# Kernel tuning notes

Hardware: AMD Instinct MI355X
Metric: run time of the kernel (lower is better)

## Reference

```python
import jax, jax.numpy as jnp
import numpy as np

B, L, H, DI, N, R, K = 1, 1024, 2048, 4096, 16, 128, 4


def setup_inputs() -> dict:
    key = jax.random.key(0)
    ks = jax.random.split(key, 12)
    s = 0.02
    x = jax.random.normal(ks[0], (B, L, H), jnp.float32)
    W_in_states = jax.random.normal(ks[1], (DI, H), jnp.float32) * s
    W_in_gates = jax.random.normal(ks[2], (DI, H), jnp.float32) * s
    conv_w = jax.random.normal(ks[3], (DI, K), jnp.float32) * 0.2
    conv_b = jax.random.normal(ks[4], (DI,), jnp.float32) * 0.02
    W_dt = jax.random.normal(ks[5], (R, DI), jnp.float32) * s
    W_b = jax.random.normal(ks[6], (N, DI), jnp.float32) * s
    W_c = jax.random.normal(ks[7], (N, DI), jnp.float32) * s
    W_dtproj = jax.random.normal(ks[8], (DI, R), jnp.float32) * 0.1
    # dt bias so softplus(dt) is in a realistic small range
    b_dtproj = jax.random.uniform(ks[9], (DI,), jnp.float32, minval=-5.0, maxval=-3.0)
    A_log = jnp.log(jnp.broadcast_to(jnp.arange(1, N + 1, dtype=jnp.float32), (DI, N)))
    D = jnp.ones((DI,), jnp.float32)
    W_out = jax.random.normal(ks[10], (H, DI), jnp.float32) * s
    return {"x": x, "W_in_states": W_in_states, "W_in_gates": W_in_gates,
            "conv_w": conv_w, "conv_b": conv_b, "W_dt": W_dt, "W_b": W_b,
            "W_c": W_c, "W_dtproj": W_dtproj, "b_dtproj": b_dtproj,
            "A_log": A_log, "D": D, "W_out": W_out}


def _silu(v):
    return v * jax.nn.sigmoid(v)


def reference(x, W_in_states, W_in_gates, conv_w, conv_b, W_dt, W_b, W_c,
              W_dtproj, b_dtproj, A_log, D, W_out):
    b, l, _ = x.shape
    # input projections -> [B, DI, L]
    hs = jnp.einsum('blh,dh->bdl', x, W_in_states)
    gate = jnp.einsum('blh,dh->bdl', x, W_in_gates)
    # causal depthwise conv1d (kernel K, left pad K-1, truncate to L)
    k = conv_w.shape[-1]
    xpad = jnp.pad(hs, ((0, 0), (0, 0), (k - 1, 0)))
    conv = sum(conv_w[None, :, j, None] * xpad[:, :, j:j + l] for j in range(k))
    conv = conv + conv_b[None, :, None]
    hs = _silu(conv)                       # [B, DI, L]
    hst = hs.transpose(0, 2, 1)            # [B, L, DI]
    # data-dependent SSM params
    time_step = jnp.einsum('bld,rd->blr', hst, W_dt)           # [B, L, R]
    dt = jax.nn.softplus(time_step @ W_dtproj.T + b_dtproj)    # [B, L, DI]
    Bm = jnp.einsum('bld,nd->bln', hst, W_b)                   # [B, L, N]
    Cm = jnp.einsum('bld,nd->bln', hst, W_c)                   # [B, L, N]
    A = -jnp.exp(A_log)                                        # [DI, N]
    dt_bdl = dt.transpose(0, 2, 1)                             # [B, DI, L]
    dA = jnp.exp(A[None, :, None, :] * dt_bdl[:, :, :, None])  # [B, DI, L, N]
    dBu = dt_bdl[:, :, :, None] * Bm[:, None, :, :] * hs[:, :, :, None]
    # sequential selective scan over L
    dA_l = dA.transpose(2, 0, 1, 3)    # [L, B, DI, N]
    dBu_l = dBu.transpose(2, 0, 1, 3)

    def step(s, inp):
        a, bu = inp
        s = a * s + bu
        return s, s

    init = jnp.zeros((b, hs.shape[1], A_log.shape[1]), hs.dtype)
    _, h = jax.lax.scan(step, init, (dA_l, dBu_l))   # [L, B, DI, N]
    y = jnp.einsum('lbdn,bln->bdl', h, Cm)           # contract state dim
    y = y + hs * D[None, :, None]
    y = y * _silu(gate)
    out = jnp.einsum('bdl,od->blo', y, W_out)        # [B, L, H]
    return out
```

## Files before the change

kernel.cpp:

```cpp
#include <hip/hip_runtime.h>

#define SEQ 1024
#define HID 2048
#define DIN 4096
#define NST 16
#define RNK 128
#define CHN 64
#define CLEN 16

typedef __attribute__((ext_vector_type(4))) float f32x4;
typedef __attribute__((ext_vector_type(4))) __bf16 bf16x4v;
typedef __attribute__((ext_vector_type(8))) __bf16 bf16x8v;
typedef __attribute__((ext_vector_type(8))) unsigned short u16x8;

#define GPTR(p) ((const __attribute__((address_space(1))) void*)(p))
#define LPTR(p) ((__attribute__((address_space(3))) void*)(p))

__device__ __forceinline__ unsigned short f2bf(float v) {
  unsigned u = __builtin_bit_cast(unsigned, v);
  u = (u + 0x7fffu + ((u >> 16) & 1u)) >> 16;
  return (unsigned short)u;
}
__device__ __forceinline__ float softplus_f(float x) {
  return (x > 20.f) ? x : log1pf(__expf(x));
}
__device__ __forceinline__ float silu_f(float x) {
  return x / (1.f + __expf(-x));
}

#define CV_NX  (SEQ*HID)
#define CV_NW  (DIN*HID)
#define CV_NDT (RNK*DIN)
#define CV_NB  (NST*DIN)
#define CV_NPD (32*DIN)
#define CV_NWO (HID*DIN)
#define CV_TOT (CV_NX + 2*CV_NW + CV_NDT + 2*CV_NB + CV_NPD + CV_NDT + CV_NWO)

__global__ __launch_bounds__(256) void cvt_all(
    const float* __restrict__ x, const float* __restrict__ wis,
    const float* __restrict__ wig, const float* __restrict__ wdt,
    const float* __restrict__ wb, const float* __restrict__ wc,
    const float* __restrict__ wdtp, const float* __restrict__ wout,
    unsigned short* __restrict__ x_bf, unsigned short* __restrict__ wis_bf,
    unsigned short* __restrict__ wig_bf, unsigned short* __restrict__ wcat_bf,
    unsigned short* __restrict__ wdtp_bf, unsigned short* __restrict__ wout_bf)
{
  size_t j = ((size_t)blockIdx.x * 256 + threadIdx.x) * 8;
  const float* src = nullptr; unsigned short* dst;
  if (j < CV_NX) { src = x + j; dst = x_bf + j; }
  else if ((j -= CV_NX) < CV_NW) { src = wis + j; dst = wis_bf + j; }
  else if ((j -= CV_NW) < CV_NW) { src = wig + j; dst = wig_bf + j; }
  else if ((j -= CV_NW) < CV_NDT) { src = wdt + j; dst = wcat_bf + j; }
  else if ((j -= CV_NDT) < CV_NB) { src = wb + j; dst = wcat_bf + (size_t)128*DIN + j; }
  else if ((j -= CV_NB) < CV_NB) { src = wc + j; dst = wcat_bf + (size_t)144*DIN + j; }
  else if ((j -= CV_NB) < CV_NPD) { dst = wcat_bf + (size_t)160*DIN + j; }
  else if ((j -= CV_NPD) < CV_NDT) { src = wdtp + j; dst = wdtp_bf + j; }
  else { j -= CV_NDT; src = wout + j; dst = wout_bf + j; }
  u16x8 o = {};
  if (src) {
    f32x4 a = *(const f32x4*)src;
    f32x4 b = *(const f32x4*)(src + 4);
#pragma unroll
    for (int i = 0; i < 4; i++) { o[i] = f2bf(a[i]); o[4 + i] = f2bf(b[i]); }
  }
  *(u16x8*)dst = o;
}

template<int EPI>
__global__ __launch_bounds__(256) void gemm128(
    const unsigned short* __restrict__ Ag, const unsigned short* __restrict__ Bg,
    float* __restrict__ Cg, const float* __restrict__ bias,
    int Msz, int Nsz, int Kstride, int Kiter)
{
  __shared__ __align__(16) unsigned short As[2][128 * 64];
  __shared__ __align__(16) unsigned short Bs[2][128 * 64];
  const int kz = blockIdx.z;
  Ag += (size_t)kz * Kiter;
  Bg += (size_t)kz * Kiter;
  Cg += (size_t)kz * Msz * Nsz;
  const int nwg = gridDim.x * gridDim.y;
  const int orig = blockIdx.y * gridDim.x + blockIdx.x;
  const int swz = (orig & 7) * (nwg >> 3) + (orig >> 3);
  const int bx = swz % gridDim.x, by = swz / gridDim.x;
  const int tid = threadIdx.x;
  const int m0 = bx * 128, n0 = by * 128;
  const int lane = tid & 63, w = tid >> 6;
  const int wm = w >> 1, wn = w & 1;
  const int lg = lane >> 4, lr = lane & 15;
  const int srow = w * 32 + (lane >> 3);
  const int sslot = (lane & 7) ^ (lane >> 3);
  const unsigned short* Ag0 = Ag + (size_t)(m0 + srow) * Kstride + sslot * 8;
  const unsigned short* Bg0 = Bg + (size_t)(n0 + srow) * Kstride + sslot * 8;
  const int ldso = w * 2048;

  auto stage = [&](int b, int k0) {
#pragma unroll
    for (int i = 0; i < 4; i++)
      __builtin_amdgcn_global_load_lds(GPTR(Ag0 + (size_t)(i * 8) * Kstride + k0),
                                       LPTR(&As[b][ldso + i * 512]), 16, 0, 0);
#pragma unroll
    for (int i = 0; i < 4; i++)
      __builtin_amdgcn_global_load_lds(GPTR(Bg0 + (size_t)(i * 8) * Kstride + k0),
                                       LPTR(&Bs[b][ldso + i * 512]), 16, 0, 0);
  };

  const int nt = Kiter >> 6;
  stage(0, 0);
  f32x4 acc[4][4] = {};
  int cur = 0;
  const int rsw = lr & 7;
  for (int t = 0; t < nt; ++t) {
    asm volatile("s_waitcnt vmcnt(0)" ::: "memory");
    __builtin_amdgcn_s_barrier();
    asm volatile("" ::: "memory");
    if (t + 1 < nt) stage(cur ^ 1, (t + 1) * 64);
    bf16x8v af0[4], bf0[4], af1[4], bf1[4];
#pragma unroll
    for (int mi = 0; mi < 4; mi++) {
      const int row = (wm * 64 + mi * 16 + lr) * 64;
      af0[mi] = *(const bf16x8v*)&As[cur][row + ((0 * 4 + lg) ^ rsw) * 8];
      af1[mi] = *(const bf16x8v*)&As[cur][row + ((1 * 4 + lg) ^ rsw) * 8];
    }
#pragma unroll
    for (int ni = 0; ni < 4; ni++) {
      const int row = (wn * 64 + ni * 16 + lr) * 64;
      bf0[ni] = *(const bf16x8v*)&Bs[cur][row + ((0 * 4 + lg) ^ rsw) * 8];
      bf1[ni] = *(const bf16x8v*)&Bs[cur][row + ((1 * 4 + lg) ^ rsw) * 8];
    }
#pragma unroll
    for (int mi = 0; mi < 4; mi++)
#pragma unroll
      for (int ni = 0; ni < 4; ni++)
        acc[mi][ni] = __builtin_amdgcn_mfma_f32_16x16x32_bf16(af0[mi], bf0[ni], acc[mi][ni], 0, 0, 0);
#pragma unroll
    for (int mi = 0; mi < 4; mi++)
#pragma unroll
      for (int ni = 0; ni < 4; ni++)
        acc[mi][ni] = __builtin_amdgcn_mfma_f32_16x16x32_bf16(af1[mi], bf1[ni], acc[mi][ni], 0, 0, 0);
    cur ^= 1;
  }
#pragma unroll
  for (int mi = 0; mi < 4; mi++) {
#pragma unroll
    for (int ni = 0; ni < 4; ni++) {
      const int col = n0 + wn * 64 + ni * 16 + lr;
#pragma unroll
      for (int r = 0; r < 4; r++) {
        const int row = m0 + wm * 64 + mi * 16 + lg * 4 + r;
        float v = acc[mi][ni][r];
        if (EPI == 1) v = softplus_f(v + bias[col]);
        Cg[(size_t)row * Nsz + col] = v;
      }
    }
  }
}

template<int EPI>
__global__ __launch_bounds__(256) void gemm_nt(
    const unsigned short* __restrict__ Ag, const unsigned short* __restrict__ Bg,
    float* __restrict__ Cg, const float* __restrict__ bias,
    int Msz, int Nsz, int Kstride, int Kiter)
{
  __shared__ __align__(16) unsigned short As[128][40];
  __shared__ __align__(16) unsigned short Bs[64][40];
  const int kz = blockIdx.z;
  Ag += (size_t)kz * Kiter;
  Bg += (size_t)kz * Kiter;
  Cg += (size_t)kz * Msz * Nsz;
  const int tid = threadIdx.x;
  const int m0 = blockIdx.x * 128, n0 = blockIdx.y * 64;
  const int lane = tid & 63, w = tid >> 6;
  const int wm = w >> 1, wn = w & 1;
  const int lg = lane >> 4, lr = lane & 15;
  const int r4 = tid >> 2, c8 = (tid & 3) * 8;
  f32x4 acc[4][2] = {};
  for (int k0 = 0; k0 < Kiter; k0 += 32) {
    uint4 a0 = *(const uint4*)(Ag + (size_t)(m0 + r4) * Kstride + k0 + c8);
    uint4 a1 = *(const uint4*)(Ag + (size_t)(m0 + 64 + r4) * Kstride + k0 + c8);
    uint4 b0 = *(const uint4*)(Bg + (size_t)(n0 + r4) * Kstride + k0 + c8);
    *(uint4*)&As[r4][c8] = a0;
    *(uint4*)&As[64 + r4][c8] = a1;
    *(uint4*)&Bs[r4][c8] = b0;
    __syncthreads();
    bf16x8v af[4], bfr[2];
#pragma unroll
    for (int mi = 0; mi < 4; mi++) {
      const int row = wm * 64 + mi * 16 + lr;
      bf16x4v lo = *(const bf16x4v*)&As[row][4 * lg];
      bf16x4v hi = *(const bf16x4v*)&As[row][16 + 4 * lg];
      af[mi] = __builtin_shufflevector(lo, hi, 0, 1, 2, 3, 4, 5, 6, 7);
    }
#pragma unroll
    for (int ni = 0; ni < 2; ni++) {
      const int row = wn * 32 + ni * 16 + lr;
      bf16x4v lo = *(const bf16x4v*)&Bs[row][4 * lg];
      bf16x4v hi = *(const bf16x4v*)&Bs[row][16 + 4 * lg];
      bfr[ni] = __builtin_shufflevector(lo, hi, 0, 1, 2, 3, 4, 5, 6, 7);
    }
#pragma unroll
    for (int mi = 0; mi < 4; mi++)
#pragma unroll
      for (int ni = 0; ni < 2; ni++)
        acc[mi][ni] = __builtin_amdgcn_mfma_f32_16x16x32_bf16(af[mi], bfr[ni], acc[mi][ni], 0, 0, 0);
    __syncthreads();
  }
#pragma unroll
  for (int mi = 0; mi < 4; mi++) {
#pragma unroll
    for (int ni = 0; ni < 2; ni++) {
      const int col = n0 + wn * 32 + ni * 16 + lr;
#pragma unroll
      for (int r = 0; r < 4; r++) {
        const int row = m0 + wm * 64 + mi * 16 + lg * 4 + r;
        float v = acc[mi][ni][r];
        if (EPI == 1) v = softplus_f(v + bias[col]);
        Cg[(size_t)row * Nsz + col] = v;
      }
    }
  }
}

__global__ __launch_bounds__(256) void conv_silu(
    const float* __restrict__ pg, const float* __restrict__ cw,
    const float* __restrict__ cb, float* __restrict__ hs,
    unsigned short* __restrict__ hs_bf)
{
  int idx = blockIdx.x * 256 + threadIdx.x;
  int l = idx >> 12, d = idx & (DIN - 1);
  float acc = cb[d];
#pragma unroll
  for (int j = 0; j < 4; j++) {
    int ll = l + j - 3;
    float v = (ll >= 0) ? pg[(size_t)ll * 8192 + d] : 0.f;
    acc = fmaf(cw[d * 4 + j], v, acc);
  }
  float r = silu_f(acc);
  hs[idx] = r;
  hs_bf[idx] = f2bf(r);
}

__global__ __launch_bounds__(256) void reduce_ts(
    const float* __restrict__ c2p, float* __restrict__ c2,
    unsigned short* __restrict__ ts_bf)
{
  int i = blockIdx.x * 256 + threadIdx.x;
  float s = 0.f;
#pragma unroll
  for (int z = 0; z < 8; z++) s += c2p[(size_t)z * SEQ * 192 + i];
  c2[i] = s;
  int l = i / 192, col = i - l * 192;
  if (col < 128) ts_bf[l * 128 + col] = f2bf(s);
}

__global__ __launch_bounds__(256) void reduce_out(
    const float* __restrict__ p, float* __restrict__ out)
{
  int i = (blockIdx.x * 256 + threadIdx.x) * 4;
  float4 a = *(const float4*)&p[i];
#pragma unroll
  for (int z = 1; z < 4; z++) {
    float4 b = *(const float4*)&p[(size_t)z * SEQ * HID + i];
    a.x += b.x; a.y += b.y; a.z += b.z; a.w += b.w;
  }
  *(float4*)&out[i] = a;
}

__global__ __launch_bounds__(256) void scan_phase1(
    const float* __restrict__ dt, const float* __restrict__ hs,
    const float* __restrict__ c2, const float* __restrict__ alog,
    float* __restrict__ Pbuf, float* __restrict__ Sbuf)
{
  __shared__ float B_ch[CLEN][16];
  const int tid = threadIdx.x;
  const int d = blockIdx.x * 256 + tid;
  const int c = blockIdx.y;
  const int l0 = c * CLEN;
  B_ch[tid >> 4][tid & 15] = c2[(size_t)(l0 + (tid >> 4)) * 192 + 128 + (tid & 15)];
  float a[16];
#pragma unroll
  for (int i = 0; i < 16; i++) a[i] = -__expf(alog[(size_t)d * 16 + i]);
  __syncthreads();
  float s[16] = {};
  float P[16];
#pragma unroll
  for (int i = 0; i < 16; i++) P[i] = 1.f;
  for (int t = 0; t < CLEN; t++) {
    float dtv = dt[(size_t)(l0 + t) * DIN + d];
    float u = hs[(size_t)(l0 + t) * DIN + d];
    float w = dtv * u;
#pragma unroll
    for (int n = 0; n < 16; n++) {
      float dA = __expf(a[n] * dtv);
      s[n] = fmaf(dA, s[n], w * B_ch[t][n]);
      P[n] *= dA;
    }
  }
  size_t base = ((size_t)c * DIN + d) * 16;
#pragma unroll
  for (int i = 0; i < 4; i++) {
    *(float4*)&Sbuf[base + 4 * i] = *(float4*)&s[4 * i];
    *(float4*)&Pbuf[base + 4 * i] = *(float4*)&P[4 * i];
  }
}

__global__ __launch_bounds__(256) void scan_phase2(
    const float* __restrict__ Pbuf, float* __restrict__ Sbuf)
{
  size_t idx = (size_t)blockIdx.x * 256 + threadIdx.x;
  const size_t stride = (size_t)DIN * 16;
  float s = 0.f;
#pragma unroll 4
  for (int c = 0; c < CHN; c++) {
    float Pv = Pbuf[c * stride + idx];
    float Sv = Sbuf[c * stride + idx];
    Sbuf[c * stride + idx] = s;
    s = fmaf(Pv, s, Sv);
  }
}

__global__ __launch_bounds__(256) void scan_phase3(
    const float* __restrict__ dt, const float* __restrict__ hs,
    const float* __restrict__ pg, const float* __restrict__ c2,
    const float* __restrict__ alog, const float* __restrict__ Dv,
    const float* __restrict__ sig, unsigned short* __restrict__ ygT)
{
  __shared__ float B_ch[CLEN][16], C_ch[CLEN][16];
  const int tid = threadIdx.x;
  const int d = blockIdx.x * 256 + tid;
  const int c = blockIdx.y;
  const int l0 = c * CLEN;
  {
    int t = tid >> 4, n = tid & 15;
    B_ch[t][n] = c2[(size_t)(l0 + t) * 192 + 128 + n];
    C_ch[t][n] = c2[(size_t)(l0 + t) * 192 + 144 + n];
  }
  float a[16];
#pragma unroll
  for (int i = 0; i < 16; i++) a[i] = -__expf(alog[(size_t)d * 16 + i]);
  const float Dd = Dv[d];
  float s[16];
  size_t base = ((size_t)c * DIN + d) * 16;
#pragma unroll
  for (int i = 0; i < 4; i++) *(float4*)&s[4 * i] = *(const float4*)&sig[base + 4 * i];
  __syncthreads();
  for (int t = 0; t < CLEN; t++) {
    float dtv = dt[(size_t)(l0 + t) * DIN + d];
    float u = hs[(size_t)(l0 + t) * DIN + d];
    float g = pg[(size_t)(l0 + t) * 8192 + 4096 + d];
    float w = dtv * u;
    float y = 0.f;
#pragma unroll
    for (int n = 0; n < 16; n++) {
      float dA = __expf(a[n] * dtv);
      s[n] = fmaf(dA, s[n], w * B_ch[t][n]);
      y = fmaf(s[n], C_ch[t][n], y);
    }
    float o = (y + u * Dd) * silu_f(g);
    ygT[(size_t)(l0 + t) * DIN + d] = f2bf(o);
  }
}

extern "C" void kernel_launch(void* const* d_in, const int* in_sizes, int n_in,
                              void* d_out, int out_size, void* d_ws, size_t ws_size,
                              hipStream_t stream) {
  const float* x     = (const float*)d_in[0];
  const float* wis   = (const float*)d_in[1];
  const float* wig   = (const float*)d_in[2];
  const float* convw = (const float*)d_in[3];
  const float* convb = (const float*)d_in[4];
  const float* wdt   = (const float*)d_in[5];
  const float* wb    = (const float*)d_in[6];
  const float* wc    = (const float*)d_in[7];
  const float* wdtp  = (const float*)d_in[8];
  const float* bdtp  = (const float*)d_in[9];
  const float* alog  = (const float*)d_in[10];
  const float* Dv    = (const float*)d_in[11];
  const float* wout  = (const float*)d_in[12];

  char* ws = (char*)d_ws;
  size_t off = 0;
  auto alloc = [&](size_t bytes) { void* p = ws + off; off += (bytes + 255) & ~(size_t)255; return p; };
  unsigned short* x_bf    = (unsigned short*)alloc((size_t)SEQ * HID * 2);
  unsigned short* wis_bf  = (unsigned short*)alloc((size_t)DIN * HID * 2);
  unsigned short* wig_bf  = (unsigned short*)alloc((size_t)DIN * HID * 2);
  unsigned short* wcat_bf = (unsigned short*)alloc((size_t)192 * DIN * 2);
  unsigned short* wdtp_bf = (unsigned short*)alloc((size_t)DIN * RNK * 2);
  unsigned short* wout_bf = (unsigned short*)alloc((size_t)HID * DIN * 2);
  float* pg    = (float*)alloc((size_t)SEQ * 8192 * 4);
  float* hs2   = (float*)alloc((size_t)SEQ * DIN * 4);
  unsigned short* hs_bf = (unsigned short*)alloc((size_t)SEQ * DIN * 2);
  float* c2    = (float*)alloc((size_t)SEQ * 192 * 4);
  float* c2p   = (float*)alloc((size_t)8 * SEQ * 192 * 4);
  unsigned short* ts_bf = (unsigned short*)alloc((size_t)SEQ * RNK * 2);
  float* dtbuf = (float*)alloc((size_t)SEQ * DIN * 4);
  unsigned short* ygT_bf = (unsigned short*)alloc((size_t)SEQ * DIN * 2);
  if (off > ws_size) return;
  float* Pbuf = (float*)wis_bf;
  float* Sbuf = (float*)wig_bf;
  float* op_part = pg;

  cvt_all<<<CV_TOT / 2048, 256, 0, stream>>>(x, wis, wig, wdt, wb, wc, wdtp, wout,
                                             x_bf, wis_bf, wig_bf, wcat_bf, wdtp_bf, wout_bf);
  gemm128<0><<<dim3(SEQ / 128, 8192 / 128), 256, 0, stream>>>(x_bf, wis_bf, pg, nullptr, SEQ, 8192, HID, HID);
  conv_silu<<<(SEQ * DIN) / 256, 256, 0, stream>>>(pg, convw, convb, hs2, hs_bf);
  gemm_nt<0><<<dim3(SEQ / 128, 192 / 64, 8), 256, 0, stream>>>(hs_bf, wcat_bf, c2p, nullptr, SEQ, 192, DIN, DIN / 8);
  reduce_ts<<<(SEQ * 192) / 256, 256, 0, stream>>>(c2p, c2, ts_bf);
  gemm_nt<1><<<dim3(SEQ / 128, DIN / 64), 256, 0, stream>>>(ts_bf, wdtp_bf, dtbuf, bdtp, SEQ, DIN, RNK, RNK);
  scan_phase1<<<dim3(DIN / 256, CHN), 256, 0, stream>>>(dtbuf, hs2, c2, alog, Pbuf, Sbuf);
  scan_phase2<<<(DIN * NST) / 256, 256, 0, stream>>>(Pbuf, Sbuf);
  scan_phase3<<<dim3(DIN / 256, CHN), 256, 0, stream>>>(dtbuf, hs2, pg, c2, alog, Dv, Sbuf, ygT_bf);
  gemm128<0><<<dim3(SEQ / 128, HID / 128, 4), 256, 0, stream>>>(ygT_bf, wout_bf, op_part, nullptr, SEQ, HID, DIN, DIN / 4);
  reduce_out<<<(SEQ * HID) / 1024, 256, 0, stream>>>(op_part, (float*)d_out);
}
```

Before: 215.5 us.

## Load GEMM A operand directly into registers, bypassing LDS

The GEMM kernel no longer stages the A tile through shared memory. Each wave loads its A fragments straight from global memory into registers, double-buffered across even and odd k-steps, while B still goes through LDS with async global-to-LDS loads. This halves LDS traffic and footprint, and a launch-bounds occupancy hint of 2 blocks per CU is added. The trade-off is redundant, less coalesced global loads for A (the two wn waves load the same rows) and higher register pressure from 16 extra bf16x8 registers.

```diff
diff --git a/kernel.cpp b/kernel.cpp
--- a/kernel.cpp
+++ b/kernel.cpp
@@ -67,12 +67,11 @@
 }
 
 template<int EPI>
-__global__ __launch_bounds__(256) void gemm128(
+__global__ __launch_bounds__(256, 2) void gemm128(
     const unsigned short* __restrict__ Ag, const unsigned short* __restrict__ Bg,
     float* __restrict__ Cg, const float* __restrict__ bias,
     int Msz, int Nsz, int Kstride, int Kiter)
 {
-  __shared__ __align__(16) unsigned short As[2][128 * 64];
   __shared__ __align__(16) unsigned short Bs[2][128 * 64];
   const int kz = blockIdx.z;
   Ag += (size_t)kz * Kiter;
@@ -89,55 +88,65 @@
   const int lg = lane >> 4, lr = lane & 15;
   const int srow = w * 32 + (lane >> 3);
   const int sslot = (lane & 7) ^ (lane >> 3);
-  const unsigned short* Ag0 = Ag + (size_t)(m0 + srow) * Kstride + sslot * 8;
   const unsigned short* Bg0 = Bg + (size_t)(n0 + srow) * Kstride + sslot * 8;
   const int ldso = w * 2048;
 
-  auto stage = [&](int b, int k0) {
-#pragma unroll
-    for (int i = 0; i < 4; i++)
-      __builtin_amdgcn_global_load_lds(GPTR(Ag0 + (size_t)(i * 8) * Kstride + k0),
-                                       LPTR(&As[b][ldso + i * 512]), 16, 0, 0);
+  auto stageB = [&](int b, int k0) {
 #pragma unroll
     for (int i = 0; i < 4; i++)
       __builtin_amdgcn_global_load_lds(GPTR(Bg0 + (size_t)(i * 8) * Kstride + k0),
                                        LPTR(&Bs[b][ldso + i * 512]), 16, 0, 0);
   };
 
+  const unsigned short* Ab = Ag + (size_t)(m0 + wm * 64 + lr) * Kstride + lg * 8;
+  auto loadA = [&](bf16x8v (&ar)[8], int k0) {
+#pragma unroll
+    for (int mi = 0; mi < 4; mi++)
+#pragma unroll
+      for (int kk = 0; kk < 2; kk++)
+        ar[mi * 2 + kk] = *(const bf16x8v*)(Ab + (size_t)(mi * 16) * Kstride + k0 + kk * 32);
+  };
+
+  const int rsw = lr & 7;
+  f32x4 acc[4][4] = {};
+
+  auto compute = [&](int b, bf16x8v (&ar)[8]) {
+    bf16x8v bf0[4], bf1[4];
+#pragma unroll
+    for (int ni = 0; ni < 4; ni++) {
+      const int row = (wn * 64 + ni * 16 + lr) * 64;
+      bf0[ni] = *(const bf16x8v*)&Bs[b][row + (lg ^ rsw) * 8];
+      bf1[ni] = *(const bf16x8v*)&Bs[b][row + ((4 + lg) ^ rsw) * 8];
+    }
+#pragma unroll
+    for (int mi = 0; mi < 4; mi++)
+#pragma unroll
+      for (int ni = 0; ni < 4; ni++)
+        acc[mi][ni] = __builtin_amdgcn_mfma_f32_16x16x32_bf16(ar[mi * 2 + 0], bf0[ni], acc[mi][ni], 0, 0, 0);
+#pragma unroll
+    for (int mi = 0; mi < 4; mi++)
+#pragma unroll
+      for (int ni = 0; ni < 4; ni++)
+        acc[mi][ni] = __builtin_amdgcn_mfma_f32_16x16x32_bf16(ar[mi * 2 + 1], bf1[ni], acc[mi][ni], 0, 0, 0);
+  };
+
   const int nt = Kiter >> 6;
-  stage(0, 0);
-  f32x4 acc[4][4] = {};
-  int cur = 0;
-  const int rsw = lr & 7;
-  for (int t = 0; t < nt; ++t) {
+  bf16x8v arE[8], arO[8];
+  stageB(0, 0);
+  loadA(arE, 0);
+  for (int t2 = 0; t2 < nt; t2 += 2) {
     asm volatile("s_waitcnt vmcnt(0)" ::: "memory");
     __builtin_amdgcn_s_barrier();
     asm volatile("" ::: "memory");
-    if (t + 1 < nt) stage(cur ^ 1, (t + 1) * 64);
-    bf16x8v af0[4], bf0[4], af1[4], bf1[4];
-#pragma unroll
-    for (int mi = 0; mi < 4; mi++) {
-      const int row = (wm * 64 + mi * 16 + lr) * 64;
-      af0[mi] = *(const bf16x8v*)&As[cur][row + ((0 * 4 + lg) ^ rsw) * 8];
-      af1[mi] = *(const bf16x8v*)&As[cur][row + ((1 * 4 + lg) ^ rsw) * 8];
-    }
-#pragma unroll
-    for (int ni = 0; ni < 4; ni++) {
-      const int row = (wn * 64 + ni * 16 + lr) * 64;
-      bf0[ni] = *(const bf16x8v*)&Bs[cur][row + ((0 * 4 + lg) ^ rsw) * 8];
-      bf1[ni] = *(const bf16x8v*)&Bs[cur][row + ((1 * 4 + lg) ^ rsw) * 8];
-    }
-#pragma unroll
-    for (int mi = 0; mi < 4; mi++)
-#pragma unroll
-      for (int ni = 0; ni < 4; ni++)
-        acc[mi][ni] = __builtin_amdgcn_mfma_f32_16x16x32_bf16(af0[mi], bf0[ni], acc[mi][ni], 0, 0, 0);
-#pragma unroll
-    for (int mi = 0; mi < 4; mi++)
-#pragma unroll
-      for (int ni = 0; ni < 4; ni++)
-        acc[mi][ni] = __builtin_amdgcn_mfma_f32_16x16x32_bf16(af1[mi], bf1[ni], acc[mi][ni], 0, 0, 0);
-    cur ^= 1;
+    if (t2 + 1 < nt) { stageB(1, (t2 + 1) * 64); loadA(arO, (t2 + 1) * 64); }
+    compute(0, arE);
+    if (t2 + 1 < nt) {
+      asm volatile("s_waitcnt vmcnt(0)" ::: "memory");
+      __builtin_amdgcn_s_barrier();
+      asm volatile("" ::: "memory");
+      if (t2 + 2 < nt) { stageB(0, (t2 + 2) * 64); loadA(arE, (t2 + 2) * 64); }
+      compute(1, arO);
+    }
   }
 #pragma unroll
   for (int mi = 0; mi < 4; mi++) {
```

After: 261.3 us. 21.3% more time.

## Convert fp32 weights to bf16 inside GEMM B-tile load instead of separate pass

Applied to the files above, without the earlier changes.

The large weight matrices (W_in_states, W_in_gates, W_out) are no longer converted to bf16 in the up-front cvt_all pass. The GEMM now loads the fp32 B tiles into registers, converts them, and writes them to LDS, with the next tile's loads issued before compute so they overlap. This removes a full read-write pass over about 64 MB of weights and frees those workspace buffers. Pbuf/Sbuf get their own allocations, and launch bounds now request 2 blocks per CU. The cost is twice the global bytes read per B tile in the GEMM, plus conversion ALU work and register pressure.

```diff
diff --git a/kernel.cpp b/kernel.cpp
--- a/kernel.cpp
+++ b/kernel.cpp
@@ -29,33 +29,26 @@
 }
 
 #define CV_NX  (SEQ*HID)
-#define CV_NW  (DIN*HID)
 #define CV_NDT (RNK*DIN)
 #define CV_NB  (NST*DIN)
 #define CV_NPD (32*DIN)
-#define CV_NWO (HID*DIN)
-#define CV_TOT (CV_NX + 2*CV_NW + CV_NDT + 2*CV_NB + CV_NPD + CV_NDT + CV_NWO)
+#define CV_TOT (CV_NX + CV_NDT + 2*CV_NB + CV_NPD + CV_NDT)
 
 __global__ __launch_bounds__(256) void cvt_all(
-    const float* __restrict__ x, const float* __restrict__ wis,
-    const float* __restrict__ wig, const float* __restrict__ wdt,
+    const float* __restrict__ x, const float* __restrict__ wdt,
     const float* __restrict__ wb, const float* __restrict__ wc,
-    const float* __restrict__ wdtp, const float* __restrict__ wout,
-    unsigned short* __restrict__ x_bf, unsigned short* __restrict__ wis_bf,
-    unsigned short* __restrict__ wig_bf, unsigned short* __restrict__ wcat_bf,
-    unsigned short* __restrict__ wdtp_bf, unsigned short* __restrict__ wout_bf)
+    const float* __restrict__ wdtp,
+    unsigned short* __restrict__ x_bf, unsigned short* __restrict__ wcat_bf,
+    unsigned short* __restrict__ wdtp_bf)
 {
   size_t j = ((size_t)blockIdx.x * 256 + threadIdx.x) * 8;
   const float* src = nullptr; unsigned short* dst;
   if (j < CV_NX) { src = x + j; dst = x_bf + j; }
-  else if ((j -= CV_NX) < CV_NW) { src = wis + j; dst = wis_bf + j; }
-  else if ((j -= CV_NW) < CV_NW) { src = wig + j; dst = wig_bf + j; }
-  else if ((j -= CV_NW) < CV_NDT) { src = wdt + j; dst = wcat_bf + j; }
+  else if ((j -= CV_NX) < CV_NDT) { src = wdt + j; dst = wcat_bf + j; }
   else if ((j -= CV_NDT) < CV_NB) { src = wb + j; dst = wcat_bf + (size_t)128*DIN + j; }
   else if ((j -= CV_NB) < CV_NB) { src = wc + j; dst = wcat_bf + (size_t)144*DIN + j; }
   else if ((j -= CV_NB) < CV_NPD) { dst = wcat_bf + (size_t)160*DIN + j; }
-  else if ((j -= CV_NPD) < CV_NDT) { src = wdtp + j; dst = wdtp_bf + j; }
-  else { j -= CV_NDT; src = wout + j; dst = wout_bf + j; }
+  else { j -= CV_NPD; src = wdtp + j; dst = wdtp_bf + j; }
   u16x8 o = {};
   if (src) {
     f32x4 a = *(const f32x4*)src;
@@ -67,8 +60,9 @@
 }
 
 template<int EPI>
-__global__ __launch_bounds__(256) void gemm128(
-    const unsigned short* __restrict__ Ag, const unsigned short* __restrict__ Bg,
+__global__ __launch_bounds__(256, 2) void gemm128(
+    const unsigned short* __restrict__ Ag,
+    const float* __restrict__ Bf0, const float* __restrict__ Bf1,
     float* __restrict__ Cg, const float* __restrict__ bias,
     int Msz, int Nsz, int Kstride, int Kiter)
 {
@@ -76,7 +70,6 @@
   __shared__ __align__(16) unsigned short Bs[2][128 * 64];
   const int kz = blockIdx.z;
   Ag += (size_t)kz * Kiter;
-  Bg += (size_t)kz * Kiter;
   Cg += (size_t)kz * Msz * Nsz;
   const int nwg = gridDim.x * gridDim.y;
   const int orig = blockIdx.y * gridDim.x + blockIdx.x;
@@ -87,45 +80,57 @@
   const int lane = tid & 63, w = tid >> 6;
   const int wm = w >> 1, wn = w & 1;
   const int lg = lane >> 4, lr = lane & 15;
+
   const int srow = w * 32 + (lane >> 3);
   const int sslot = (lane & 7) ^ (lane >> 3);
   const unsigned short* Ag0 = Ag + (size_t)(m0 + srow) * Kstride + sslot * 8;
-  const unsigned short* Bg0 = Bg + (size_t)(n0 + srow) * Kstride + sslot * 8;
   const int ldso = w * 2048;
-
-  auto stage = [&](int b, int k0) {
+  auto stageA = [&](int b, int k0) {
 #pragma unroll
     for (int i = 0; i < 4; i++)
       __builtin_amdgcn_global_load_lds(GPTR(Ag0 + (size_t)(i * 8) * Kstride + k0),
                                        LPTR(&As[b][ldso + i * 512]), 16, 0, 0);
-#pragma unroll
-    for (int i = 0; i < 4; i++)
-      __builtin_amdgcn_global_load_lds(GPTR(Bg0 + (size_t)(i * 8) * Kstride + k0),
-                                       LPTR(&Bs[b][ldso + i * 512]), 16, 0, 0);
   };
 
-  const int nt = Kiter >> 6;
-  stage(0, 0);
+  const int brow = tid >> 1;
+  const int c0 = (tid & 1) * 4;
+  const float* Bbase = (n0 < 4096) ? (Bf0 + (size_t)n0 * Kstride)
+                                   : (Bf1 + (size_t)(n0 - 4096) * Kstride);
+  const float* Brow = Bbase + (size_t)brow * Kstride + (tid & 1) * 32 + (size_t)kz * Kiter;
+  const int bws = brow & 7;
+
+  f32x4 ld[8];
+  auto loadB = [&](int k0) {
+#pragma unroll
+    for (int j = 0; j < 8; j++) ld[j] = *(const f32x4*)(Brow + k0 + j * 4);
+  };
+  auto writeB = [&](int b) {
+#pragma unroll
+    for (int j = 0; j < 4; j++) {
+      bf16x8v v;
+      v[0] = (__bf16)ld[2 * j][0]; v[1] = (__bf16)ld[2 * j][1];
+      v[2] = (__bf16)ld[2 * j][2]; v[3] = (__bf16)ld[2 * j][3];
+      v[4] = (__bf16)ld[2 * j + 1][0]; v[5] = (__bf16)ld[2 * j + 1][1];
+      v[6] = (__bf16)ld[2 * j + 1][2]; v[7] = (__bf16)ld[2 * j + 1][3];
+      *(bf16x8v*)&Bs[b][brow * 64 + ((c0 + j) ^ bws) * 8] = v;
+    }
+  };
+
+  const int rsw = lr & 7;
   f32x4 acc[4][4] = {};
-  int cur = 0;
-  const int rsw = lr & 7;
-  for (int t = 0; t < nt; ++t) {
-    asm volatile("s_waitcnt vmcnt(0)" ::: "memory");
-    __builtin_amdgcn_s_barrier();
-    asm volatile("" ::: "memory");
-    if (t + 1 < nt) stage(cur ^ 1, (t + 1) * 64);
-    bf16x8v af0[4], bf0[4], af1[4], bf1[4];
+  auto compute = [&](int b) {
+    bf16x8v af0[4], af1[4], bf0[4], bf1[4];
 #pragma unroll
     for (int mi = 0; mi < 4; mi++) {
       const int row = (wm * 64 + mi * 16 + lr) * 64;
-      af0[mi] = *(const bf16x8v*)&As[cur][row + ((0 * 4 + lg) ^ rsw) * 8];
-      af1[mi] = *(const bf16x8v*)&As[cur][row + ((1 * 4 + lg) ^ rsw) * 8];
+      af0[mi] = *(const bf16x8v*)&As[b][row + (lg ^ rsw) * 8];
+      af1[mi] = *(const bf16x8v*)&As[b][row + ((4 + lg) ^ rsw) * 8];
     }
 #pragma unroll
     for (int ni = 0; ni < 4; ni++) {
       const int row = (wn * 64 + ni * 16 + lr) * 64;
-      bf0[ni] = *(const bf16x8v*)&Bs[cur][row + ((0 * 4 + lg) ^ rsw) * 8];
-      bf1[ni] = *(const bf16x8v*)&Bs[cur][row + ((1 * 4 + lg) ^ rsw) * 8];
+      bf0[ni] = *(const bf16x8v*)&Bs[b][row + (lg ^ rsw) * 8];
+      bf1[ni] = *(const bf16x8v*)&Bs[b][row + ((4 + lg) ^ rsw) * 8];
     }
 #pragma unroll
     for (int mi = 0; mi < 4; mi++)
@@ -137,6 +142,19 @@
 #pragma unroll
       for (int ni = 0; ni < 4; ni++)
         acc[mi][ni] = __builtin_amdgcn_mfma_f32_16x16x32_bf16(af1[mi], bf1[ni], acc[mi][ni], 0, 0, 0);
+  };
+
+  const int nt = Kiter >> 6;
+  stageA(0, 0);
+  loadB(0);
+  writeB(0);
+  __syncthreads();
+  int cur = 0;
+  for (int t = 0; t < nt; ++t) {
+    if (t + 1 < nt) { stageA(cur ^ 1, (t + 1) * 64); loadB((t + 1) * 64); }
+    compute(cur);
+    if (t + 1 < nt) writeB(cur ^ 1);
+    __syncthreads();
     cur ^= 1;
   }
 #pragma unroll
@@ -381,11 +399,8 @@
   size_t off = 0;
   auto alloc = [&](size_t bytes) { void* p = ws + off; off += (bytes + 255) & ~(size_t)255; return p; };
   unsigned short* x_bf    = (unsigned short*)alloc((size_t)SEQ * HID * 2);
-  unsigned short* wis_bf  = (unsigned short*)alloc((size_t)DIN * HID * 2);
-  unsigned short* wig_bf  = (unsigned short*)alloc((size_t)DIN * HID * 2);
   unsigned short* wcat_bf = (unsigned short*)alloc((size_t)192 * DIN * 2);
   unsigned short* wdtp_bf = (unsigned short*)alloc((size_t)DIN * RNK * 2);
-  unsigned short* wout_bf = (unsigned short*)alloc((size_t)HID * DIN * 2);
   float* pg    = (float*)alloc((size_t)SEQ * 8192 * 4);
   float* hs2   = (float*)alloc((size_t)SEQ * DIN * 4);
   unsigned short* hs_bf = (unsigned short*)alloc((size_t)SEQ * DIN * 2);
@@ -394,14 +409,14 @@
   unsigned short* ts_bf = (unsigned short*)alloc((size_t)SEQ * RNK * 2);
   float* dtbuf = (float*)alloc((size_t)SEQ * DIN * 4);
   unsigned short* ygT_bf = (unsigned short*)alloc((size_t)SEQ * DIN * 2);
+  float* Pbuf  = (float*)alloc((size_t)CHN * DIN * NST * 4);
+  float* Sbuf  = (float*)alloc((size_t)CHN * DIN * NST * 4);
   if (off > ws_size) return;
-  float* Pbuf = (float*)wis_bf;
-  float* Sbuf = (float*)wig_bf;
   float* op_part = pg;
 
-  cvt_all<<<CV_TOT / 2048, 256, 0, stream>>>(x, wis, wig, wdt, wb, wc, wdtp, wout,
-                                             x_bf, wis_bf, wig_bf, wcat_bf, wdtp_bf, wout_bf);
-  gemm128<0><<<dim3(SEQ / 128, 8192 / 128), 256, 0, stream>>>(x_bf, wis_bf, pg, nullptr, SEQ, 8192, HID, HID);
+  cvt_all<<<CV_TOT / 2048, 256, 0, stream>>>(x, wdt, wb, wc, wdtp,
+                                             x_bf, wcat_bf, wdtp_bf);
+  gemm128<0><<<dim3(SEQ / 128, 8192 / 128), 256, 0, stream>>>(x_bf, wis, wig, pg, nullptr, SEQ, 8192, HID, HID);
   conv_silu<<<(SEQ * DIN) / 256, 256, 0, stream>>>(pg, convw, convb, hs2, hs_bf);
   gemm_nt<0><<<dim3(SEQ / 128, 192 / 64, 8), 256, 0, stream>>>(hs_bf, wcat_bf, c2p, nullptr, SEQ, 192, DIN, DIN / 8);
   reduce_ts<<<(SEQ * 192) / 256, 256, 0, stream>>>(c2p, c2, ts_bf);
@@ -409,6 +424,6 @@
   scan_phase1<<<dim3(DIN / 256, CHN), 256, 0, stream>>>(dtbuf, hs2, c2, alog, Pbuf, Sbuf);
   scan_phase2<<<(DIN * NST) / 256, 256, 0, stream>>>(Pbuf, Sbuf);
   scan_phase3<<<dim3(DIN / 256, CHN), 256, 0, stream>>>(dtbuf, hs2, pg, c2, alog, Dv, Sbuf, ygT_bf);
-  gemm128<0><<<dim3(SEQ / 128, HID / 128, 4), 256, 0, stream>>>(ygT_bf, wout_bf, op_part, nullptr, SEQ, HID, DIN, DIN / 4);
+  gemm128<0><<<dim3(SEQ / 128, HID / 128, 4), 256, 0, stream>>>(ygT_bf, wout, wout, op_part, nullptr, SEQ, HID, DIN, DIN / 4);
   reduce_out<<<(SEQ * HID) / 1024, 256, 0, stream>>>(op_part, (float*)d_out);
 }
```

New measurement: 246.5 us. 1.14x slower.
